# Optimization experiments

Hardware: AMD Instinct MI355X
Metric: run time of the kernel (lower is better)

## Reference

```python
import jax, jax.numpy as jnp
import numpy as np

EMB_SIZE = 256  # VQ embedding_size
BETA = 0.25     # commitment cost


def _mlp(x, W1, b1, W2, b2, W3, b3):
    h = jax.nn.relu(x @ W1 + b1)
    h = jax.nn.relu(h @ W2 + b2)
    return h @ W3 + b3


def setup_inputs() -> dict:
    key = jax.random.key(0)
    ks = jax.random.split(key, 5)
    B, D = 1024, 1024
    s = 1.0 / np.sqrt(D)
    return {
        "observation": jax.random.normal(ks[0], (B, D), jnp.float32),
        "W1": jax.random.normal(ks[1], (D, D), jnp.float32) * s,
        "b1": jnp.zeros((D,), jnp.float32),
        "W2": jax.random.normal(ks[2], (D, D), jnp.float32) * s,
        "b2": jnp.zeros((D,), jnp.float32),
        "W3": jax.random.normal(ks[3], (D, D), jnp.float32) * s,
        "b3": jnp.zeros((D,), jnp.float32),
        "codebook": jax.random.normal(ks[4], (512, EMB_SIZE), jnp.float32),
    }


def reference(observation, W1, b1, W2, b2, W3, b3, codebook):
    # Dense encoder
    features = _mlp(observation, W1, b1, W2, b2, W3, b3)  # [B, 1024]
    # Flatten features into embedding_size-dim tokens: [B*4, 256]
    z = features.reshape(-1, EMB_SIZE)
    # Squared euclidean distances to codebook: [N, K]
    d = (jnp.sum(z * z, axis=1, keepdims=True)
         - 2.0 * (z @ codebook.T)
         + jnp.sum(codebook * codebook, axis=1)[None, :])
    idx = jnp.argmin(d, axis=1)                   # [N] nearest code indices
    quantized = codebook[idx]                     # [N, 256] gather
    # VQ losses
    commitment_loss = jnp.mean((jax.lax.stop_gradient(quantized) - z) ** 2)
    codebook_loss = jnp.mean((quantized - jax.lax.stop_gradient(z)) ** 2)
    loss = codebook_loss + BETA * commitment_loss
    # Straight-through estimator
    quantized_st = z + jax.lax.stop_gradient(quantized - z)
    out = quantized_st.reshape(features.shape)    # [B, 1024]
    return out, loss, idx
```

## Files before the change

### kernel.cpp

```cpp
#include <hip/hip_runtime.h>


typedef _Float16 half8 __attribute__((ext_vector_type(8)));
typedef _Float16 half4 __attribute__((ext_vector_type(4)));
typedef float floatx4 __attribute__((ext_vector_type(4)));

#define LO_SCALE 2048.0f
#define INV_LO_SCALE (1.0f / 2048.0f)

__device__ __forceinline__ int remap4(int k0)
{
    return (k0 & 32) | ((k0 & 12) << 1) | ((k0 & 16) >> 2);
}
__device__ __forceinline__ int remap1(int k)
{
    return (k & ~63) | (k & 32) | ((k & 12) << 1) | ((k & 16) >> 2) | (k & 3);
}

__device__ __forceinline__ void gl_lds16(const _Float16* g, _Float16* l)
{
    __builtin_amdgcn_global_load_lds(
        (const __attribute__((address_space(1))) void*)g,
        (__attribute__((address_space(3))) void*)l, 16, 0, 0);
}

__device__ __forceinline__ half8 rfrag(const _Float16* m, int row, int ks, int fg)
{
    const int ch = ((ks << 2) + fg) ^ (row & 7);
    return *reinterpret_cast<const half8*>(&m[(row << 6) + (ch << 3)]);
}

template <bool RELU, bool WSPLIT, bool ARGMIN>
__global__ __launch_bounds__(256) void gemm_k(
    const _Float16* __restrict__ Ah, const _Float16* __restrict__ Al,
    const _Float16* __restrict__ Bh, const _Float16* __restrict__ Bl,
    const float* __restrict__ bias,
    _Float16* __restrict__ Ch, _Float16* __restrict__ Cl,
    const float* __restrict__ cnorm, float* __restrict__ pv, int* __restrict__ pi,
    int N, int K)
{
    __shared__ __align__(16) _Float16 sm[2][4][4096];

    const int tid = threadIdx.x;
    const int m0 = blockIdx.y * 64, n0 = blockIdx.x * 64;
    const int w = tid >> 6, lane = tid & 63;
    const int srow = lane >> 3, sc = lane & 7;

    const _Float16* gsrc = (w == 0) ? Ah : (w == 1) ? Al : (w == 2) ? Bh : Bl;
    const int rb0 = (w < 2) ? m0 : n0;
    const size_t gbase = (size_t)(rb0 + srow) * K + ((sc ^ srow) << 3);

    const int wm = (w & 1) * 32, wn = (w >> 1) * 32;
    const int fr = lane & 15, fg = lane >> 4;

    floatx4 hh[2][2] = {};
    floatx4 c1[2][2] = {};
    floatx4 c2[2][2] = {};

    const int NT = K >> 6;

    auto STAGE = [&](int buf, int t) {
        const size_t kb = (size_t)(t << 6);
        #pragma unroll
        for (int j = 0; j < 8; ++j)
            gl_lds16(gsrc + gbase + (size_t)(j << 3) * K + kb,
                     &sm[buf][w][(j << 3) << 6]);
    };

    STAGE(0, 0);
    __syncthreads();

    for (int t = 0; t < NT; ++t) {
        const int cur = t & 1;
        if (t + 1 < NT) STAGE(cur ^ 1, t + 1);
        #pragma unroll
        for (int ks = 0; ks < 2; ++ks) {
            half8 a_h[2], a_l[2], b_h[2], b_l[2];
            #pragma unroll
            for (int i = 0; i < 2; ++i) {
                a_h[i] = rfrag(sm[cur][0], wm + (i << 4) + fr, ks, fg);
                a_l[i] = rfrag(sm[cur][1], wm + (i << 4) + fr, ks, fg);
                b_h[i] = rfrag(sm[cur][2], wn + (i << 4) + fr, ks, fg);
                b_l[i] = rfrag(sm[cur][3], wn + (i << 4) + fr, ks, fg);
            }
            #pragma unroll
            for (int i = 0; i < 2; ++i)
                #pragma unroll
                for (int j = 0; j < 2; ++j) {
                    hh[i][j] = __builtin_amdgcn_mfma_f32_16x16x32_f16(a_h[i], b_h[j], hh[i][j], 0, 0, 0);
                    c1[i][j] = __builtin_amdgcn_mfma_f32_16x16x32_f16(a_h[i], b_l[j], c1[i][j], 0, 0, 0);
                    c2[i][j] = __builtin_amdgcn_mfma_f32_16x16x32_f16(a_l[i], b_h[j], c2[i][j], 0, 0, 0);
                }
        }
        __syncthreads();
    }

    if (!ARGMIN) {
        #pragma unroll
        for (int j = 0; j < 2; ++j) {
            const int col = n0 + wn + (j << 4) + fr;
            const float bv = bias ? bias[col] : 0.0f;
            const int colr = remap1(col);
            #pragma unroll
            for (int i = 0; i < 2; ++i)
                #pragma unroll
                for (int r = 0; r < 4; ++r) {
                    const int row = m0 + wm + (i << 4) + (fg << 2) + r;
                    float v = hh[i][j][r] + (c1[i][j][r] + c2[i][j][r]) * INV_LO_SCALE + bv;
                    if (RELU) v = fmaxf(v, 0.0f);
                    if (WSPLIT) {
                        const size_t o = (size_t)row * N + colr;
                        const _Float16 hi = (_Float16)v;
                        Ch[o] = hi;
                        Cl[o] = (_Float16)((v - (float)hi) * LO_SCALE);
                    }
                }
        }
    } else {
        const int cA = n0 + wn + fr, cB = cA + 16;
        const float cnA = cnorm[cA], cnB = cnorm[cB];
        float* cv = (float*)&sm[0][0][0];
        int* ci = (int*)(cv + 128);
        #pragma unroll
        for (int i = 0; i < 2; ++i)
            #pragma unroll
            for (int r = 0; r < 4; ++r) {
                const float v0 = hh[i][0][r] + (c1[i][0][r] + c2[i][0][r]) * INV_LO_SCALE;
                const float v1 = hh[i][1][r] + (c1[i][1][r] + c2[i][1][r]) * INV_LO_SCALE;
                const float d0 = fmaf(-2.0f, v0, cnA);
                const float d1 = fmaf(-2.0f, v1, cnB);
                float d = d0; int di = cA;
                if (d1 < d0) { d = d1; di = cB; }
                #pragma unroll
                for (int msk = 1; msk <= 8; msk <<= 1) {
                    const float ov = __shfl_xor(d, msk);
                    const int oi = __shfl_xor(di, msk);
                    if (ov < d || (ov == d && oi < di)) { d = ov; di = oi; }
                }
                if (fr == 0) {
                    const int rl = (i << 4) + (fg << 2) + r;
                    cv[w * 32 + rl] = d;
                    ci[w * 32 + rl] = di;
                }
            }
        __syncthreads();
        if (tid < 64) {
            const int a = tid >> 5, rl = tid & 31;
            float d = cv[a * 32 + rl]; int di = ci[a * 32 + rl];
            const float d2 = cv[(a + 2) * 32 + rl];
            const int i2 = ci[(a + 2) * 32 + rl];
            if (d2 < d || (d2 == d && i2 < di)) { d = d2; di = i2; }
            pv[blockIdx.x * 4096 + m0 + tid] = d;
            pi[blockIdx.x * 4096 + m0 + tid] = di;
        }
    }
}

__global__ __launch_bounds__(256) void prep_kernel(
    const float* __restrict__ W1, const float* __restrict__ W2,
    const float* __restrict__ W3, const float* __restrict__ obs,
    const float* __restrict__ CB,
    _Float16* __restrict__ T1h, _Float16* __restrict__ T1l,
    _Float16* __restrict__ T2h, _Float16* __restrict__ T2l,
    _Float16* __restrict__ T3h, _Float16* __restrict__ T3l,
    _Float16* __restrict__ Oh, _Float16* __restrict__ Ol,
    _Float16* __restrict__ CBh, _Float16* __restrict__ CBl,
    float* __restrict__ cnorm)
{
    __shared__ float tile[64][65];
    const int b = blockIdx.x, tid = threadIdx.x;

    if (b < 768) {
        const int z = b >> 8, rem = b & 255;
        const float* Wm = (z == 0) ? W1 : (z == 1) ? W2 : W3;
        _Float16* Th = (z == 0) ? T1h : (z == 1) ? T2h : T3h;
        _Float16* Tl = (z == 0) ? T1l : (z == 1) ? T2l : T3l;
        const int nb = (rem & 15) * 64, kb = (rem >> 4) * 64;
        {
            const int kr = tid >> 2, c0 = (tid & 3) * 16;
            #pragma unroll
            for (int c = 0; c < 16; c += 4) {
                float4 v = *reinterpret_cast<const float4*>(
                    &Wm[(size_t)(kb + kr) * 1024 + nb + c0 + c]);
                tile[kr][c0 + c] = v.x; tile[kr][c0 + c + 1] = v.y;
                tile[kr][c0 + c + 2] = v.z; tile[kr][c0 + c + 3] = v.w;
            }
        }
        __syncthreads();
        {
            const int nr = tid >> 2, k0 = (tid & 3) * 16;
            #pragma unroll
            for (int g = 0; g < 4; ++g) {
                const int kk = k0 + g * 4;
                half4 h, lo;
                #pragma unroll
                for (int j = 0; j < 4; ++j) {
                    const float x = tile[kk + j][nr];
                    const _Float16 hi = (_Float16)x;
                    h[j] = hi;
                    lo[j] = (_Float16)((x - (float)hi) * LO_SCALE);
                }
                const size_t o = (size_t)(nb + nr) * 1024 + kb + remap4(kk);
                *reinterpret_cast<half4*>(&Th[o]) = h;
                *reinterpret_cast<half4*>(&Tl[o]) = lo;
            }
        }
    } else if (b < 1280) {
        const size_t e0 = ((size_t)(b - 768) * 256 + tid) * 8;
        float4 a = *reinterpret_cast<const float4*>(&obs[e0]);
        float4 c = *reinterpret_cast<const float4*>(&obs[e0 + 4]);
        float xs[8] = {a.x, a.y, a.z, a.w, c.x, c.y, c.z, c.w};
        half4 h[2], lo[2];
        #pragma unroll
        for (int q = 0; q < 2; ++q)
            #pragma unroll
            for (int j = 0; j < 4; ++j) {
                const float x = xs[q * 4 + j];
                const _Float16 hi = (_Float16)x;
                h[q][j] = hi;
                lo[q][j] = (_Float16)((x - (float)hi) * LO_SCALE);
            }
        const size_t base = e0 & ~(size_t)63;
        const int r1 = remap4((int)(e0 & 63));
        const int r2 = remap4((int)((e0 + 4) & 63));
        *reinterpret_cast<half4*>(&Oh[base + r1]) = h[0];
        *reinterpret_cast<half4*>(&Oh[base + r2]) = h[1];
        *reinterpret_cast<half4*>(&Ol[base + r1]) = lo[0];
        *reinterpret_cast<half4*>(&Ol[base + r2]) = lo[1];
    } else {
        const int wv = tid >> 6, lane = tid & 63;
        const int code = (b - 1280) * 4 + wv;
        const int k0 = lane * 4;
        float4 c = *reinterpret_cast<const float4*>(&CB[(size_t)code * 256 + k0]);
        float xs[4] = {c.x, c.y, c.z, c.w};
        half4 h, lo;
        float s = 0.f;
        #pragma unroll
        for (int j = 0; j < 4; ++j) {
            const _Float16 hi = (_Float16)xs[j];
            h[j] = hi;
            lo[j] = (_Float16)((xs[j] - (float)hi) * LO_SCALE);
            s += xs[j] * xs[j];
        }
        const size_t o = (size_t)code * 256 + (k0 & ~63) + remap4(k0 & 63);
        *reinterpret_cast<half4*>(&CBh[o]) = h;
        *reinterpret_cast<half4*>(&CBl[o]) = lo;
        #pragma unroll
        for (int off = 32; off; off >>= 1) s += __shfl_down(s, off);
        if (lane == 0) cnorm[code] = s;
    }
}

__global__ __launch_bounds__(512) void vq_lite_kernel(
    const float* __restrict__ pv, const int* __restrict__ pi,
    const _Float16* __restrict__ Fh, const _Float16* __restrict__ Fl,
    const float* __restrict__ CB,
    float* __restrict__ out, float* __restrict__ pl, float* __restrict__ idx_out)
{
    const int wid = threadIdx.x >> 6, lane = threadIdx.x & 63;
    const int n = blockIdx.x * 8 + wid;

    float best = 3.4e38f;
    int bidx = 0x7fffffff;
    if (lane < 8) { best = pv[lane * 4096 + n]; bidx = pi[lane * 4096 + n]; }
    #pragma unroll
    for (int msk = 1; msk <= 4; msk <<= 1) {
        const float ov = __shfl_xor(best, msk);
        const int oi = __shfl_xor(bidx, msk);
        if (ov < best || (ov == best && oi < bidx)) { best = ov; bidx = oi; }
    }
    bidx = __shfl(bidx, 0);
    best = __shfl(best, 0);

    const int base = n * 256 + lane * 4;
    half4 h4 = *reinterpret_cast<const half4*>(&Fh[base]);
    half4 l4 = *reinterpret_cast<const half4*>(&Fl[base]);
    float zn = 0.f;
    #pragma unroll
    for (int j = 0; j < 4; ++j) {
        const float z = (float)h4[j] + (float)l4[j] * INV_LO_SCALE;
        zn = fmaf(z, z, zn);
    }
    #pragma unroll
    for (int off = 32; off; off >>= 1) zn += __shfl_down(zn, off);

    float4 q4 = *reinterpret_cast<const float4*>(&CB[(size_t)bidx * 256 + lane * 4]);
    *reinterpret_cast<float4*>(&out[(size_t)n * 256 + lane * 4]) = q4;

    __shared__ float part[8];
    if (lane == 0) {
        part[wid] = zn + best;
        idx_out[n] = (float)bidx;
    }
    __syncthreads();
    if (threadIdx.x == 0) {
        float s = 0.f;
        #pragma unroll
        for (int i = 0; i < 8; ++i) s += part[i];
        pl[blockIdx.x] = s;
    }
}

__global__ __launch_bounds__(512) void finalize_kernel(
    const float* __restrict__ pl, float* __restrict__ loss_out)
{
    float s = pl[threadIdx.x];
    #pragma unroll
    for (int off = 32; off; off >>= 1) s += __shfl_down(s, off);
    __shared__ float p[8];
    if ((threadIdx.x & 63) == 0) p[threadIdx.x >> 6] = s;
    __syncthreads();
    if (threadIdx.x == 0) {
        float t = 0.f;
        #pragma unroll
        for (int i = 0; i < 8; ++i) t += p[i];
        loss_out[0] = 1.25f * t / 1048576.0f;
    }
}

extern "C" void kernel_launch(void* const* d_in, const int* in_sizes, int n_in,
                              void* d_out, int out_size, void* d_ws, size_t ws_size,
                              hipStream_t stream)
{
    const float* obs = (const float*)d_in[0];
    const float* W1  = (const float*)d_in[1];
    const float* b1  = (const float*)d_in[2];
    const float* W2  = (const float*)d_in[3];
    const float* b2  = (const float*)d_in[4];
    const float* W3  = (const float*)d_in[5];
    const float* b3  = (const float*)d_in[6];
    const float* CB  = (const float*)d_in[7];

    float* out = (float*)d_out;
    float* loss_out = out + 1048576;
    float* idx_out  = out + 1048577;

    char* Wp = (char*)d_ws;
    _Float16* Oh    = (_Float16*)(Wp + (0u  << 20));
    _Float16* Ol    = (_Float16*)(Wp + (2u  << 20));
    _Float16* W1t_h = (_Float16*)(Wp + (4u  << 20));
    _Float16* W1t_l = (_Float16*)(Wp + (6u  << 20));
    _Float16* W2t_h = (_Float16*)(Wp + (8u  << 20));
    _Float16* W2t_l = (_Float16*)(Wp + (10u << 20));
    _Float16* W3t_h = (_Float16*)(Wp + (12u << 20));
    _Float16* W3t_l = (_Float16*)(Wp + (14u << 20));
    _Float16* H1_h  = (_Float16*)(Wp + (16u << 20));
    _Float16* H1_l  = (_Float16*)(Wp + (18u << 20));
    _Float16* H2_h  = (_Float16*)(Wp + (20u << 20));
    _Float16* H2_l  = (_Float16*)(Wp + (22u << 20));
    _Float16* F_h   = (_Float16*)(Wp + (24u << 20));
    _Float16* F_l   = (_Float16*)(Wp + (26u << 20));
    _Float16* CB_h  = (_Float16*)(Wp + (28u << 20));
    _Float16* CB_l  = (_Float16*)(Wp + (28u << 20) + 512 * 256 * 2);
    float*    cn    = (float*)(Wp + (28u << 20) + 2 * 512 * 256 * 2);
    float*    pv    = (float*)(Wp + (29u << 20));
    int*      pi    = (int*)(Wp + (30u << 20));
    float*    pl    = (float*)(Wp + (31u << 20));

    prep_kernel<<<1408, 256, 0, stream>>>(
        W1, W2, W3, obs, CB,
        W1t_h, W1t_l, W2t_h, W2t_l, W3t_h, W3t_l,
        Oh, Ol, CB_h, CB_l, cn);

    gemm_k<true, true, false><<<dim3(16, 16), 256, 0, stream>>>(
        Oh, Ol, W1t_h, W1t_l, b1, H1_h, H1_l, nullptr, nullptr, nullptr, 1024, 1024);
    gemm_k<true, true, false><<<dim3(16, 16), 256, 0, stream>>>(
        H1_h, H1_l, W2t_h, W2t_l, b2, H2_h, H2_l, nullptr, nullptr, nullptr, 1024, 1024);
    gemm_k<false, true, false><<<dim3(16, 16), 256, 0, stream>>>(
        H2_h, H2_l, W3t_h, W3t_l, b3, F_h, F_l, nullptr, nullptr, nullptr, 1024, 1024);

    gemm_k<false, false, true><<<dim3(8, 64), 256, 0, stream>>>(
        F_h, F_l, CB_h, CB_l, nullptr, nullptr, nullptr, cn, pv, pi, 512, 256);

    vq_lite_kernel<<<512, 512, 0, stream>>>(pv, pi, F_h, F_l, CB, out, pl, idx_out);
    finalize_kernel<<<1, 512, 0, stream>>>(pl, loss_out);
}
```

Before: 141.2 us.

## Fuse all stages into one persistent cooperative kernel with grid syncs

```diff
diff --git a/kernel.cpp b/kernel.cpp
--- a/kernel.cpp
+++ b/kernel.cpp
@@ -1,4 +1,7 @@
 #include <hip/hip_runtime.h>
+#include <hip/hip_cooperative_groups.h>
+
+namespace cg = cooperative_groups;
 
 
 typedef _Float16 half8 __attribute__((ext_vector_type(8)));
@@ -31,7 +34,8 @@
 }
 
 template <bool RELU, bool WSPLIT, bool ARGMIN>
-__global__ __launch_bounds__(256) void gemm_k(
+__device__ void gemm_phase(
+    unsigned char* smem, int tile, int nTilesX,
     const _Float16* __restrict__ Ah, const _Float16* __restrict__ Al,
     const _Float16* __restrict__ Bh, const _Float16* __restrict__ Bl,
     const float* __restrict__ bias,
@@ -39,10 +43,11 @@
     const float* __restrict__ cnorm, float* __restrict__ pv, int* __restrict__ pi,
     int N, int K)
 {
-    __shared__ __align__(16) _Float16 sm[2][4][4096];
+    _Float16* smh = (_Float16*)smem;
 
     const int tid = threadIdx.x;
-    const int m0 = blockIdx.y * 64, n0 = blockIdx.x * 64;
+    const int cbx = tile % nTilesX;
+    const int m0 = (tile / nTilesX) * 64, n0 = cbx * 64;
     const int w = tid >> 6, lane = tid & 63;
     const int srow = lane >> 3, sc = lane & 7;
 
@@ -61,27 +66,29 @@
 
     auto STAGE = [&](int buf, int t) {
         const size_t kb = (size_t)(t << 6);
+        _Float16* dst = smh + buf * 16384 + w * 4096;
         #pragma unroll
         for (int j = 0; j < 8; ++j)
-            gl_lds16(gsrc + gbase + (size_t)(j << 3) * K + kb,
-                     &sm[buf][w][(j << 3) << 6]);
+            gl_lds16(gsrc + gbase + (size_t)(j << 3) * K + kb, dst + (j << 9));
     };
 
+    __syncthreads();
     STAGE(0, 0);
     __syncthreads();
 
     for (int t = 0; t < NT; ++t) {
         const int cur = t & 1;
         if (t + 1 < NT) STAGE(cur ^ 1, t + 1);
+        const _Float16* s0 = smh + cur * 16384;
         #pragma unroll
         for (int ks = 0; ks < 2; ++ks) {
             half8 a_h[2], a_l[2], b_h[2], b_l[2];
             #pragma unroll
             for (int i = 0; i < 2; ++i) {
-                a_h[i] = rfrag(sm[cur][0], wm + (i << 4) + fr, ks, fg);
-                a_l[i] = rfrag(sm[cur][1], wm + (i << 4) + fr, ks, fg);
-                b_h[i] = rfrag(sm[cur][2], wn + (i << 4) + fr, ks, fg);
-                b_l[i] = rfrag(sm[cur][3], wn + (i << 4) + fr, ks, fg);
+                a_h[i] = rfrag(s0,          wm + (i << 4) + fr, ks, fg);
+                a_l[i] = rfrag(s0 + 4096,   wm + (i << 4) + fr, ks, fg);
+                b_h[i] = rfrag(s0 + 8192,   wn + (i << 4) + fr, ks, fg);
+                b_l[i] = rfrag(s0 + 12288,  wn + (i << 4) + fr, ks, fg);
             }
             #pragma unroll
             for (int i = 0; i < 2; ++i)
@@ -119,7 +126,7 @@
     } else {
         const int cA = n0 + wn + fr, cB = cA + 16;
         const float cnA = cnorm[cA], cnB = cnorm[cB];
-        float* cv = (float*)&sm[0][0][0];
+        float* cv = (float*)smem;
         int* ci = (int*)(cv + 128);
         #pragma unroll
         for (int i = 0; i < 2; ++i)
@@ -150,13 +157,14 @@
             const float d2 = cv[(a + 2) * 32 + rl];
             const int i2 = ci[(a + 2) * 32 + rl];
             if (d2 < d || (d2 == d && i2 < di)) { d = d2; di = i2; }
-            pv[blockIdx.x * 4096 + m0 + tid] = d;
-            pi[blockIdx.x * 4096 + m0 + tid] = di;
-        }
-    }
-}
-
-__global__ __launch_bounds__(256) void prep_kernel(
+            pv[cbx * 4096 + m0 + tid] = d;
+            pi[cbx * 4096 + m0 + tid] = di;
+        }
+    }
+}
+
+__device__ void prep_task(
+    unsigned char* smem, int task,
     const float* __restrict__ W1, const float* __restrict__ W2,
     const float* __restrict__ W3, const float* __restrict__ obs,
     const float* __restrict__ CB,
@@ -167,11 +175,10 @@
     _Float16* __restrict__ CBh, _Float16* __restrict__ CBl,
     float* __restrict__ cnorm)
 {
-    __shared__ float tile[64][65];
-    const int b = blockIdx.x, tid = threadIdx.x;
-
-    if (b < 768) {
-        const int z = b >> 8, rem = b & 255;
+    const int tid = threadIdx.x;
+    if (task < 768) {
+        float (*tile)[65] = reinterpret_cast<float(*)[65]>(smem);
+        const int z = task >> 8, rem = task & 255;
         const float* Wm = (z == 0) ? W1 : (z == 1) ? W2 : W3;
         _Float16* Th = (z == 0) ? T1h : (z == 1) ? T2h : T3h;
         _Float16* Tl = (z == 0) ? T1l : (z == 1) ? T2l : T3l;
@@ -205,8 +212,8 @@
                 *reinterpret_cast<half4*>(&Tl[o]) = lo;
             }
         }
-    } else if (b < 1280) {
-        const size_t e0 = ((size_t)(b - 768) * 256 + tid) * 8;
+    } else if (task < 1280) {
+        const size_t e0 = ((size_t)(task - 768) * 256 + tid) * 8;
         float4 a = *reinterpret_cast<const float4*>(&obs[e0]);
         float4 c = *reinterpret_cast<const float4*>(&obs[e0 + 4]);
         float xs[8] = {a.x, a.y, a.z, a.w, c.x, c.y, c.z, c.w};
@@ -229,7 +236,7 @@
         *reinterpret_cast<half4*>(&Ol[base + r2]) = lo[1];
     } else {
         const int wv = tid >> 6, lane = tid & 63;
-        const int code = (b - 1280) * 4 + wv;
+        const int code = (task - 1280) * 4 + wv;
         const int k0 = lane * 4;
         float4 c = *reinterpret_cast<const float4*>(&CB[(size_t)code * 256 + k0]);
         float xs[4] = {c.x, c.y, c.z, c.w};
@@ -251,71 +258,137 @@
     }
 }
 
-__global__ __launch_bounds__(512) void vq_lite_kernel(
+__device__ void vq_phase(
+    unsigned char* smem, int bid, int NB,
     const float* __restrict__ pv, const int* __restrict__ pi,
     const _Float16* __restrict__ Fh, const _Float16* __restrict__ Fl,
     const float* __restrict__ CB,
-    float* __restrict__ out, float* __restrict__ pl, float* __restrict__ idx_out)
-{
-    const int wid = threadIdx.x >> 6, lane = threadIdx.x & 63;
-    const int n = blockIdx.x * 8 + wid;
-
-    float best = 3.4e38f;
-    int bidx = 0x7fffffff;
-    if (lane < 8) { best = pv[lane * 4096 + n]; bidx = pi[lane * 4096 + n]; }
-    #pragma unroll
-    for (int msk = 1; msk <= 4; msk <<= 1) {
-        const float ov = __shfl_xor(best, msk);
-        const int oi = __shfl_xor(bidx, msk);
-        if (ov < best || (ov == best && oi < bidx)) { best = ov; bidx = oi; }
-    }
-    bidx = __shfl(bidx, 0);
-    best = __shfl(best, 0);
-
-    const int base = n * 256 + lane * 4;
-    half4 h4 = *reinterpret_cast<const half4*>(&Fh[base]);
-    half4 l4 = *reinterpret_cast<const half4*>(&Fl[base]);
-    float zn = 0.f;
-    #pragma unroll
-    for (int j = 0; j < 4; ++j) {
-        const float z = (float)h4[j] + (float)l4[j] * INV_LO_SCALE;
-        zn = fmaf(z, z, zn);
-    }
-    #pragma unroll
-    for (int off = 32; off; off >>= 1) zn += __shfl_down(zn, off);
-
-    float4 q4 = *reinterpret_cast<const float4*>(&CB[(size_t)bidx * 256 + lane * 4]);
-    *reinterpret_cast<float4*>(&out[(size_t)n * 256 + lane * 4]) = q4;
-
-    __shared__ float part[8];
-    if (lane == 0) {
-        part[wid] = zn + best;
-        idx_out[n] = (float)bidx;
-    }
-    __syncthreads();
-    if (threadIdx.x == 0) {
-        float s = 0.f;
-        #pragma unroll
-        for (int i = 0; i < 8; ++i) s += part[i];
-        pl[blockIdx.x] = s;
-    }
-}
-
-__global__ __launch_bounds__(512) void finalize_kernel(
-    const float* __restrict__ pl, float* __restrict__ loss_out)
-{
-    float s = pl[threadIdx.x];
-    #pragma unroll
-    for (int off = 32; off; off >>= 1) s += __shfl_down(s, off);
-    __shared__ float p[8];
-    if ((threadIdx.x & 63) == 0) p[threadIdx.x >> 6] = s;
-    __syncthreads();
-    if (threadIdx.x == 0) {
-        float t = 0.f;
-        #pragma unroll
-        for (int i = 0; i < 8; ++i) t += p[i];
-        loss_out[0] = 1.25f * t / 1048576.0f;
-    }
+    float* __restrict__ out, float* __restrict__ loss_out,
+    float* __restrict__ idx_out)
+{
+    const int tid = threadIdx.x, wid = tid >> 6, lane = tid & 63;
+    float* part = (float*)smem;
+    float acc = 0.f;
+
+    for (int n0 = bid * 4; n0 < 4096; n0 += NB * 4) {
+        const int n = n0 + wid;
+        float best = 3.4e38f;
+        int bidx = 0x7fffffff;
+        if (lane < 8) { best = pv[lane * 4096 + n]; bidx = pi[lane * 4096 + n]; }
+        #pragma unroll
+        for (int msk = 1; msk <= 4; msk <<= 1) {
+            const float ov = __shfl_xor(best, msk);
+            const int oi = __shfl_xor(bidx, msk);
+            if (ov < best || (ov == best && oi < bidx)) { best = ov; bidx = oi; }
+        }
+        bidx = __shfl(bidx, 0);
+        best = __shfl(best, 0);
+
+        const int base = n * 256 + lane * 4;
+        half4 h4 = *reinterpret_cast<const half4*>(&Fh[base]);
+        half4 l4 = *reinterpret_cast<const half4*>(&Fl[base]);
+        float zn = 0.f;
+        #pragma unroll
+        for (int j = 0; j < 4; ++j) {
+            const float z = (float)h4[j] + (float)l4[j] * INV_LO_SCALE;
+            zn = fmaf(z, z, zn);
+        }
+        #pragma unroll
+        for (int off = 32; off; off >>= 1) zn += __shfl_down(zn, off);
+
+        float4 q4 = *reinterpret_cast<const float4*>(&CB[(size_t)bidx * 256 + lane * 4]);
+        *reinterpret_cast<float4*>(&out[(size_t)n * 256 + lane * 4]) = q4;
+
+        __syncthreads();
+        if (lane == 0) {
+            part[wid] = zn + best;
+            idx_out[n] = (float)bidx;
+        }
+        __syncthreads();
+        if (tid == 0) acc += part[0] + part[1] + part[2] + part[3];
+    }
+    if (tid == 0) atomicAdd(loss_out, acc * (1.25f / 1048576.0f));
+}
+
+__global__ __launch_bounds__(256) void mega_kernel(
+    const float* obs, const float* W1, const float* b1,
+    const float* W2, const float* b2, const float* W3, const float* b3,
+    const float* CB,
+    _Float16* Oh, _Float16* Ol,
+    _Float16* T1h, _Float16* T1l, _Float16* T2h, _Float16* T2l,
+    _Float16* T3h, _Float16* T3l,
+    _Float16* H1h, _Float16* H1l, _Float16* H2h, _Float16* H2l,
+    _Float16* Fh, _Float16* Fl,
+    _Float16* CBh, _Float16* CBl, float* cn, float* pv, int* pi,
+    float* out, float* loss_out, float* idx_out)
+{
+    __shared__ __align__(16) unsigned char smem[65536];
+    cg::grid_group grid = cg::this_grid();
+    const int bid = blockIdx.x, NB = gridDim.x;
+
+    for (int task = bid; task < 1408; task += NB) {
+        __syncthreads();
+        prep_task(smem, task, W1, W2, W3, obs, CB,
+                  T1h, T1l, T2h, T2l, T3h, T3l, Oh, Ol, CBh, CBl, cn);
+    }
+    if (bid == 0 && threadIdx.x == 0) loss_out[0] = 0.f;
+    grid.sync();
+
+    for (int t = bid; t < 256; t += NB)
+        gemm_phase<true, true, false>(smem, t, 16, Oh, Ol, T1h, T1l, b1,
+                                      H1h, H1l, nullptr, nullptr, nullptr, 1024, 1024);
+    grid.sync();
+    for (int t = bid; t < 256; t += NB)
+        gemm_phase<true, true, false>(smem, t, 16, H1h, H1l, T2h, T2l, b2,
+                                      H2h, H2l, nullptr, nullptr, nullptr, 1024, 1024);
+    grid.sync();
+    for (int t = bid; t < 256; t += NB)
+        gemm_phase<false, true, false>(smem, t, 16, H2h, H2l, T3h, T3l, b3,
+                                       Fh, Fl, nullptr, nullptr, nullptr, 1024, 1024);
+    grid.sync();
+
+    for (int t = bid; t < 512; t += NB)
+        gemm_phase<false, false, true>(smem, t, 8, Fh, Fl, CBh, CBl, nullptr,
+                                       nullptr, nullptr, cn, pv, pi, 512, 256);
+    grid.sync();
+
+    vq_phase(smem, bid, NB, pv, pi, Fh, Fl, CB, out, loss_out, idx_out);
+}
+
+__global__ __launch_bounds__(256) void prep_g(
+    const float* W1, const float* W2, const float* W3,
+    const float* obs, const float* CB,
+    _Float16* T1h, _Float16* T1l, _Float16* T2h, _Float16* T2l,
+    _Float16* T3h, _Float16* T3l,
+    _Float16* Oh, _Float16* Ol, _Float16* CBh, _Float16* CBl,
+    float* cn, float* loss_out)
+{
+    __shared__ __align__(16) unsigned char smem[64 * 65 * 4];
+    prep_task(smem, blockIdx.x, W1, W2, W3, obs, CB,
+              T1h, T1l, T2h, T2l, T3h, T3l, Oh, Ol, CBh, CBl, cn);
+    if (blockIdx.x == 0 && threadIdx.x == 0) loss_out[0] = 0.f;
+}
+
+template <bool RELU, bool WSPLIT, bool ARGMIN>
+__global__ __launch_bounds__(256) void gemm_g(
+    const _Float16* Ah, const _Float16* Al,
+    const _Float16* Bh, const _Float16* Bl, const float* bias,
+    _Float16* Ch, _Float16* Cl,
+    const float* cnorm, float* pv, int* pi, int nTilesX, int N, int K)
+{
+    __shared__ __align__(16) unsigned char smem[65536];
+    gemm_phase<RELU, WSPLIT, ARGMIN>(smem, blockIdx.x, nTilesX,
+                                     Ah, Al, Bh, Bl, bias, Ch, Cl,
+                                     cnorm, pv, pi, N, K);
+}
+
+__global__ __launch_bounds__(256) void vq_g(
+    const float* pv, const int* pi, const _Float16* Fh, const _Float16* Fl,
+    const float* CB, float* out, float* loss_out, float* idx_out)
+{
+    __shared__ __align__(16) unsigned char smem[64];
+    vq_phase(smem, blockIdx.x, gridDim.x, pv, pi, Fh, Fl, CB,
+             out, loss_out, idx_out);
 }
 
 extern "C" void kernel_launch(void* const* d_in, const int* in_sizes, int n_in,
@@ -355,23 +428,46 @@
     float*    cn    = (float*)(Wp + (28u << 20) + 2 * 512 * 256 * 2);
     float*    pv    = (float*)(Wp + (29u << 20));
     int*      pi    = (int*)(Wp + (30u << 20));
-    float*    pl    = (float*)(Wp + (31u << 20));
-
-    prep_kernel<<<1408, 256, 0, stream>>>(
-        W1, W2, W3, obs, CB,
-        W1t_h, W1t_l, W2t_h, W2t_l, W3t_h, W3t_l,
-        Oh, Ol, CB_h, CB_l, cn);
-
-    gemm_k<true, true, false><<<dim3(16, 16), 256, 0, stream>>>(
-        Oh, Ol, W1t_h, W1t_l, b1, H1_h, H1_l, nullptr, nullptr, nullptr, 1024, 1024);
-    gemm_k<true, true, false><<<dim3(16, 16), 256, 0, stream>>>(
-        H1_h, H1_l, W2t_h, W2t_l, b2, H2_h, H2_l, nullptr, nullptr, nullptr, 1024, 1024);
-    gemm_k<false, true, false><<<dim3(16, 16), 256, 0, stream>>>(
-        H2_h, H2_l, W3t_h, W3t_l, b3, F_h, F_l, nullptr, nullptr, nullptr, 1024, 1024);
-
-    gemm_k<false, false, true><<<dim3(8, 64), 256, 0, stream>>>(
-        F_h, F_l, CB_h, CB_l, nullptr, nullptr, nullptr, cn, pv, pi, 512, 256);
-
-    vq_lite_kernel<<<512, 512, 0, stream>>>(pv, pi, F_h, F_l, CB, out, pl, idx_out);
-    finalize_kernel<<<1, 512, 0, stream>>>(pl, loss_out);
-}
+
+    int occ = 0;
+    hipError_t e = hipOccupancyMaxActiveBlocksPerMultiprocessor(
+        &occ, (const void*)mega_kernel, 256, 0);
+    bool coop = (e == hipSuccess && occ >= 1);
+    if (coop) {
+        void* args[] = {
+            (void*)&obs, (void*)&W1, (void*)&b1, (void*)&W2, (void*)&b2,
+            (void*)&W3, (void*)&b3, (void*)&CB,
+            (void*)&Oh, (void*)&Ol,
+            (void*)&W1t_h, (void*)&W1t_l, (void*)&W2t_h, (void*)&W2t_l,
+            (void*)&W3t_h, (void*)&W3t_l,
+            (void*)&H1_h, (void*)&H1_l, (void*)&H2_h, (void*)&H2_l,
+            (void*)&F_h, (void*)&F_l,
+            (void*)&CB_h, (void*)&CB_l, (void*)&cn, (void*)&pv, (void*)&pi,
+            (void*)&out, (void*)&loss_out, (void*)&idx_out,
+        };
+        e = hipLaunchCooperativeKernel((const void*)mega_kernel,
+                                       dim3(256), dim3(256), args, 0, stream);
+        coop = (e == hipSuccess);
+    }
+
+    if (!coop) {
+        prep_g<<<1408, 256, 0, stream>>>(
+            W1, W2, W3, obs, CB,
+            W1t_h, W1t_l, W2t_h, W2t_l, W3t_h, W3t_l,
+            Oh, Ol, CB_h, CB_l, cn, loss_out);
+        gemm_g<true, true, false><<<256, 256, 0, stream>>>(
+            Oh, Ol, W1t_h, W1t_l, b1, H1_h, H1_l,
+            nullptr, nullptr, nullptr, 16, 1024, 1024);
+        gemm_g<true, true, false><<<256, 256, 0, stream>>>(
+            H1_h, H1_l, W2t_h, W2t_l, b2, H2_h, H2_l,
+            nullptr, nullptr, nullptr, 16, 1024, 1024);
+        gemm_g<false, true, false><<<256, 256, 0, stream>>>(
+            H2_h, H2_l, W3t_h, W3t_l, b3, F_h, F_l,
+            nullptr, nullptr, nullptr, 16, 1024, 1024);
+        gemm_g<false, false, true><<<512, 256, 0, stream>>>(
+            F_h, F_l, CB_h, CB_l, nullptr, nullptr, nullptr,
+            cn, pv, pi, 8, 512, 256);
+        vq_g<<<1024, 256, 0, stream>>>(pv, pi, F_h, F_l, CB,
+                                       out, loss_out, idx_out);
+    }
+}
```

After: 319.0 us. 126% more time.
